# Kernel optimization log

Hardware: AMD Instinct MI355X
Metric: run time of the kernel (lower is better)

## Reference

```python
import jax, jax.numpy as jnp
import numpy as np

EPS = 1e-6

def _normalize(A):
    # zero the diagonal, add self-loops
    n = A.shape[-1]
    eye = jnp.eye(n, dtype=A.dtype)
    A_hat = A * (1.0 - eye) + eye  # [B,N,N]
    # symmetric degree normalization with eps inside as in the TF code:
    # d = 1/(eps + sqrt(rowsum)); norm = diag(d) @ A_hat @ diag(d)
    d = 1.0 / (EPS + jnp.sqrt(jnp.sum(A_hat, axis=2)))  # [B,N]
    return A_hat * d[:, :, None] * d[:, None, :]


def setup_inputs() -> dict:
    key = jax.random.key(0)
    k1, k2, k3 = jax.random.split(key, 3)
    B, N, F, O = 8, 2048, 128, 128
    x = jax.random.normal(k1, (B, N, F), dtype=jnp.float32)
    adj = jax.random.uniform(k2, (B, N, N), dtype=jnp.float32)
    kernel = jax.random.normal(k3, (F, O), dtype=jnp.float32) * 0.05
    return {"x": x, "adj": adj, "kernel": kernel}


def reference(x, adj, kernel):
    norm = _normalize(adj)                      # [B,N,N]
    agg = jnp.einsum('bnm,bmf->bnf', norm, x)   # batch_dot
    out = jnp.einsum('bnf,fo->bno', agg, kernel)
    return jax.nn.relu(out)
```

## Files before the change

kernel.cpp:

```cpp
#include <hip/hip_runtime.h>


typedef __bf16 bf16x8 __attribute__((ext_vector_type(8)));
typedef float  f32x4  __attribute__((ext_vector_type(4)));

#define NN 2048
#define NB 8

__device__ __forceinline__ void load_lds16(__bf16* lds, const __bf16* g) {
    __builtin_amdgcn_global_load_lds(
        (const __attribute__((address_space(1))) void*)g,
        (__attribute__((address_space(3))) void*)lds, 16, 0, 0);
}

__global__ __launch_bounds__(256) void d_kernel(const float* __restrict__ adj,
                                                float* __restrict__ dvec,
                                                const float* __restrict__ W,
                                                __bf16* __restrict__ Wt) {
    if (blockIdx.x >= NB * NN / 4) {
        int idx = (blockIdx.x - NB * NN / 4) * 256 + threadIdx.x;
        int f = idx >> 7, o = idx & 127;
        Wt[o * 128 + f] = (__bf16)W[idx];
        return;
    }
    const int lane = threadIdx.x & 63;
    const int row  = blockIdx.x * 4 + (threadIdx.x >> 6);
    const float* rp = adj + (size_t)row * NN;
    float4 s4 = {0.f, 0.f, 0.f, 0.f};
#pragma unroll
    for (int it = 0; it < 8; ++it) {
        float4 v = *(const float4*)(rp + it * 256 + lane * 4);
        s4.x += v.x; s4.y += v.y; s4.z += v.z; s4.w += v.w;
    }
    float s = (s4.x + s4.y) + (s4.z + s4.w);
#pragma unroll
    for (int off = 32; off; off >>= 1) s += __shfl_down(s, off);
    if (lane == 0) {
        int n = row & (NN - 1);
        float sh = s - rp[n] + 1.0f;
        dvec[row] = 1.0f / (1e-6f + sqrtf(sh));
    }
}

__global__ __launch_bounds__(256) void xw_kernel(const float* __restrict__ x,
                                                 const __bf16* __restrict__ Wt,
                                                 const float* __restrict__ dvec,
                                                 __bf16* __restrict__ yt) {
    const int lane = threadIdx.x & 63;
    const int wave = threadIdx.x >> 6;
    const int b    = blockIdx.x & 7;
    const int mt   = (blockIdx.x >> 3) * 4 + wave;
    const int m0   = mt * 16;
    const int kgrp = (lane >> 4) * 8;
    const float* xp = x + ((size_t)b * NN + m0 + (lane & 15)) * 128 + kgrp;

    f32x4 acc[8];
#pragma unroll
    for (int i = 0; i < 8; ++i) acc[i] = (f32x4){0.f, 0.f, 0.f, 0.f};

#pragma unroll
    for (int kt = 0; kt < 4; ++kt) {
        f32x4 a0 = *(const f32x4*)(xp + kt * 32);
        f32x4 a1 = *(const f32x4*)(xp + kt * 32 + 4);
        float av[8] = {a0.x, a0.y, a0.z, a0.w, a1.x, a1.y, a1.z, a1.w};
        bf16x8 af;
#pragma unroll
        for (int j = 0; j < 8; ++j) af[j] = (__bf16)av[j];
#pragma unroll
        for (int nb = 0; nb < 8; ++nb) {
            bf16x8 bfv = *(const bf16x8*)(Wt + (nb * 16 + (lane & 15)) * 128 +
                                          kt * 32 + kgrp);
            acc[nb] = __builtin_amdgcn_mfma_f32_16x16x32_bf16(af, bfv, acc[nb], 0, 0, 0);
        }
    }
    const int col0 = lane & 15;
    const int rq   = (lane >> 4) * 4;
#pragma unroll
    for (int r = 0; r < 4; ++r) {
        int m = m0 + rq + r;
        float dm = dvec[b * NN + m];
#pragma unroll
        for (int nb = 0; nb < 8; ++nb) {
            int o = nb * 16 + col0;
            yt[((size_t)b * 128 + o) * NN + m] = (__bf16)(acc[nb][r] * dm);
        }
    }
}

__global__ __launch_bounds__(256) void gemm_kernel(const float* __restrict__ adj,
                                                   const __bf16* __restrict__ yt,
                                                   const float* __restrict__ dvec,
                                                   float* __restrict__ out) {
    __shared__ alignas(16) __bf16 sB[2][128][32];

    const int tid  = threadIdx.x;
    const int wave = tid >> 6;
    const int lane = tid & 63;
    const int b    = blockIdx.x & 7;
    const int tile = blockIdx.x >> 3;
    const int rsel = (wave & 1) * 16;
    const int csel = (wave >> 1) * 64;
    const int kgrp = (lane >> 4) * 8;

    const int arow_loc = tile * 32 + rsel + (lane & 15);
    const float* ap = adj + ((size_t)b * NN + arow_loc) * NN + kgrp;

    const __bf16* ytb = yt + (size_t)b * 128 * NN;
    const int b_row0 = wave * 32;
    const __bf16* b_src = ytb + (size_t)(b_row0 + (lane >> 2)) * NN + (lane & 3) * 8;

    f32x4 acc[4];
#pragma unroll
    for (int i = 0; i < 4; ++i) acc[i] = (f32x4){0.f, 0.f, 0.f, 0.f};

    load_lds16(&sB[0][b_row0][0], b_src);
    load_lds16(&sB[0][b_row0 + 16][0], b_src + (size_t)16 * NN);
    __builtin_amdgcn_sched_barrier(0);
    f32x4 ca0 = *(const f32x4*)(ap);
    f32x4 ca1 = *(const f32x4*)(ap + 4);

    for (int kt = 0; kt < 64; ++kt) {
        const int cur = kt & 1;
        asm volatile("s_waitcnt vmcnt(2)" ::: "memory");
        __builtin_amdgcn_sched_barrier(0);
        __builtin_amdgcn_s_barrier();
        __builtin_amdgcn_sched_barrier(0);

        f32x4 na0, na1;
        if (kt + 1 < 64) {
            const __bf16* bs = b_src + (size_t)(kt + 1) * 32;
            load_lds16(&sB[cur ^ 1][b_row0][0], bs);
            load_lds16(&sB[cur ^ 1][b_row0 + 16][0], bs + (size_t)16 * NN);
            __builtin_amdgcn_sched_barrier(0);
            na0 = *(const f32x4*)(ap + (kt + 1) * 32);
            na1 = *(const f32x4*)(ap + (kt + 1) * 32 + 4);
        }

        bf16x8 af;
        af[0] = (__bf16)ca0.x; af[1] = (__bf16)ca0.y;
        af[2] = (__bf16)ca0.z; af[3] = (__bf16)ca0.w;
        af[4] = (__bf16)ca1.x; af[5] = (__bf16)ca1.y;
        af[6] = (__bf16)ca1.z; af[7] = (__bf16)ca1.w;

#pragma unroll
        for (int nb = 0; nb < 4; ++nb) {
            bf16x8 bfv = *(const bf16x8*)(
                &sB[cur][csel + nb * 16 + (lane & 15)][kgrp]);
            acc[nb] = __builtin_amdgcn_mfma_f32_16x16x32_bf16(af, bfv, acc[nb], 0, 0, 0);
        }
        ca0 = na0; ca1 = na1;
    }

    const int col0 = lane & 15;
    const int rq   = (lane >> 4) * 4;
#pragma unroll
    for (int r = 0; r < 4; ++r) {
        int n_loc = tile * 32 + rsel + rq + r;
        size_t grow = (size_t)b * NN + n_loc;
        float dn   = dvec[grow];
        float cfac = 1.0f - adj[grow * NN + n_loc];
#pragma unroll
        for (int nb = 0; nb < 4; ++nb) {
            int o = csel + nb * 16 + col0;
            float yp = (float)ytb[(size_t)o * NN + n_loc];
            float v = (acc[nb][r] + cfac * yp) * dn;
            out[grow * 128 + o] = v > 0.f ? v : 0.f;
        }
    }
}

extern "C" void kernel_launch(void* const* d_in, const int* in_sizes, int n_in,
                              void* d_out, int out_size, void* d_ws, size_t ws_size,
                              hipStream_t stream) {
    const float* x   = (const float*)d_in[0];
    const float* adj = (const float*)d_in[1];
    const float* W   = (const float*)d_in[2];
    float* out = (float*)d_out;

    char* ws = (char*)d_ws;
    float*  dvec = (float*)ws;
    __bf16* Wt   = (__bf16*)(ws + (64 << 10));
    __bf16* yt   = (__bf16*)(ws + (128 << 10));

    hipLaunchKernelGGL(d_kernel, dim3(NB * NN / 4 + 64), dim3(256), 0, stream,
                       adj, dvec, W, Wt);
    hipLaunchKernelGGL(xw_kernel, dim3(256), dim3(256), 0, stream, x, Wt, dvec, yt);
    hipLaunchKernelGGL(gemm_kernel, dim3(512), dim3(256), 0, stream,
                       adj, yt, dvec, out);
}
```

Before: 246.5 us.

## Deepen gemm pipeline to 4-stage LDS ring with 2-ahead A prefetch

The main GEMM loop moves from a double-buffered LDS scheme to a 4-slot ring that issues B tile loads three iterations ahead and A register loads two iterations ahead. The loop is manually unrolled by two so the A prefetch registers alternate, and the waitcnt thresholds are tuned for the tail iterations. The intent is to keep more memory requests in flight and hide global latency behind MFMA work, at the cost of more LDS and registers per block.

```diff
diff --git a/kernel.cpp b/kernel.cpp
--- a/kernel.cpp
+++ b/kernel.cpp
@@ -87,11 +87,46 @@
     }
 }
 
+
+#define GBODY(KT, S, DO_A, DO_G, WAITSTR)                                    \
+  do {                                                                       \
+    asm volatile("s_waitcnt vmcnt(" WAITSTR ")" ::: "memory");               \
+    __builtin_amdgcn_sched_barrier(0);                                       \
+    __builtin_amdgcn_s_barrier();                                            \
+    __builtin_amdgcn_sched_barrier(0);                                       \
+    const int cur_ = (KT) & 3;                                               \
+    bf16x8 bv0 = *(const bf16x8*)(&sB[cur_][csel +  0 + l15][kgrp]);         \
+    bf16x8 bv1 = *(const bf16x8*)(&sB[cur_][csel + 16 + l15][kgrp]);         \
+    bf16x8 bv2 = *(const bf16x8*)(&sB[cur_][csel + 32 + l15][kgrp]);         \
+    bf16x8 bv3 = *(const bf16x8*)(&sB[cur_][csel + 48 + l15][kgrp]);         \
+    bf16x8 af;                                                               \
+    af[0] = (__bf16)pa0_##S.x; af[1] = (__bf16)pa0_##S.y;                    \
+    af[2] = (__bf16)pa0_##S.z; af[3] = (__bf16)pa0_##S.w;                    \
+    af[4] = (__bf16)pa1_##S.x; af[5] = (__bf16)pa1_##S.y;                    \
+    af[6] = (__bf16)pa1_##S.z; af[7] = (__bf16)pa1_##S.w;                    \
+    __builtin_amdgcn_sched_barrier(0);                                       \
+    if (DO_A) {                                                              \
+      pa0_##S = *(const f32x4*)(ap + ((KT) + 2) * 32);                       \
+      pa1_##S = *(const f32x4*)(ap + ((KT) + 2) * 32 + 4);                   \
+    }                                                                        \
+    __builtin_amdgcn_sched_barrier(0);                                       \
+    if (DO_G) {                                                              \
+      const __bf16* bs_ = b_src + (size_t)((KT) + 3) * 32;                   \
+      load_lds16(&sB[((KT) + 3) & 3][b_row0][0], bs_);                       \
+      load_lds16(&sB[((KT) + 3) & 3][b_row0 + 16][0], bs_ + (size_t)16 * NN);\
+    }                                                                        \
+    __builtin_amdgcn_sched_barrier(0);                                       \
+    acc[0] = __builtin_amdgcn_mfma_f32_16x16x32_bf16(af, bv0, acc[0], 0, 0, 0); \
+    acc[1] = __builtin_amdgcn_mfma_f32_16x16x32_bf16(af, bv1, acc[1], 0, 0, 0); \
+    acc[2] = __builtin_amdgcn_mfma_f32_16x16x32_bf16(af, bv2, acc[2], 0, 0, 0); \
+    acc[3] = __builtin_amdgcn_mfma_f32_16x16x32_bf16(af, bv3, acc[3], 0, 0, 0); \
+  } while (0)
+
 __global__ __launch_bounds__(256) void gemm_kernel(const float* __restrict__ adj,
                                                    const __bf16* __restrict__ yt,
                                                    const float* __restrict__ dvec,
                                                    float* __restrict__ out) {
-    __shared__ alignas(16) __bf16 sB[2][128][32];
+    __shared__ alignas(16) __bf16 sB[4][128][32];
 
     const int tid  = threadIdx.x;
     const int wave = tid >> 6;
@@ -101,8 +136,9 @@
     const int rsel = (wave & 1) * 16;
     const int csel = (wave >> 1) * 64;
     const int kgrp = (lane >> 4) * 8;
-
-    const int arow_loc = tile * 32 + rsel + (lane & 15);
+    const int l15  = lane & 15;
+
+    const int arow_loc = tile * 32 + rsel + l15;
     const float* ap = adj + ((size_t)b * NN + arow_loc) * NN + kgrp;
 
     const __bf16* ytb = yt + (size_t)b * 128 * NN;
@@ -113,46 +149,34 @@
 #pragma unroll
     for (int i = 0; i < 4; ++i) acc[i] = (f32x4){0.f, 0.f, 0.f, 0.f};
 
+    f32x4 pa0_0, pa1_0, pa0_1, pa1_1;
+
     load_lds16(&sB[0][b_row0][0], b_src);
     load_lds16(&sB[0][b_row0 + 16][0], b_src + (size_t)16 * NN);
     __builtin_amdgcn_sched_barrier(0);
-    f32x4 ca0 = *(const f32x4*)(ap);
-    f32x4 ca1 = *(const f32x4*)(ap + 4);
-
-    for (int kt = 0; kt < 64; ++kt) {
-        const int cur = kt & 1;
-        asm volatile("s_waitcnt vmcnt(2)" ::: "memory");
-        __builtin_amdgcn_sched_barrier(0);
-        __builtin_amdgcn_s_barrier();
-        __builtin_amdgcn_sched_barrier(0);
-
-        f32x4 na0, na1;
-        if (kt + 1 < 64) {
-            const __bf16* bs = b_src + (size_t)(kt + 1) * 32;
-            load_lds16(&sB[cur ^ 1][b_row0][0], bs);
-            load_lds16(&sB[cur ^ 1][b_row0 + 16][0], bs + (size_t)16 * NN);
-            __builtin_amdgcn_sched_barrier(0);
-            na0 = *(const f32x4*)(ap + (kt + 1) * 32);
-            na1 = *(const f32x4*)(ap + (kt + 1) * 32 + 4);
-        }
-
-        bf16x8 af;
-        af[0] = (__bf16)ca0.x; af[1] = (__bf16)ca0.y;
-        af[2] = (__bf16)ca0.z; af[3] = (__bf16)ca0.w;
-        af[4] = (__bf16)ca1.x; af[5] = (__bf16)ca1.y;
-        af[6] = (__bf16)ca1.z; af[7] = (__bf16)ca1.w;
-
-#pragma unroll
-        for (int nb = 0; nb < 4; ++nb) {
-            bf16x8 bfv = *(const bf16x8*)(
-                &sB[cur][csel + nb * 16 + (lane & 15)][kgrp]);
-            acc[nb] = __builtin_amdgcn_mfma_f32_16x16x32_bf16(af, bfv, acc[nb], 0, 0, 0);
-        }
-        ca0 = na0; ca1 = na1;
-    }
-
-    const int col0 = lane & 15;
-    const int rq   = (lane >> 4) * 4;
+    pa0_0 = *(const f32x4*)(ap);
+    pa1_0 = *(const f32x4*)(ap + 4);
+    __builtin_amdgcn_sched_barrier(0);
+    load_lds16(&sB[1][b_row0][0], b_src + 32);
+    load_lds16(&sB[1][b_row0 + 16][0], b_src + (size_t)16 * NN + 32);
+    __builtin_amdgcn_sched_barrier(0);
+    pa0_1 = *(const f32x4*)(ap + 32);
+    pa1_1 = *(const f32x4*)(ap + 36);
+    __builtin_amdgcn_sched_barrier(0);
+    load_lds16(&sB[2][b_row0][0], b_src + 64);
+    load_lds16(&sB[2][b_row0 + 16][0], b_src + (size_t)16 * NN + 64);
+    __builtin_amdgcn_sched_barrier(0);
+
+    for (int kt = 0; kt < 60; kt += 2) {
+        GBODY(kt,     0, 1, 1, "6");
+        GBODY(kt + 1, 1, 1, 1, "6");
+    }
+    GBODY(60, 0, 1, 1, "6");
+    GBODY(61, 1, 1, 0, "6");
+    GBODY(62, 0, 0, 0, "4");
+    GBODY(63, 1, 0, 0, "0");
+
+    const int rq = (lane >> 4) * 4;
 #pragma unroll
     for (int r = 0; r < 4; ++r) {
         int n_loc = tile * 32 + rsel + rq + r;
@@ -161,7 +185,7 @@
         float cfac = 1.0f - adj[grow * NN + n_loc];
 #pragma unroll
         for (int nb = 0; nb < 4; ++nb) {
-            int o = csel + nb * 16 + col0;
+            int o = csel + nb * 16 + l15;
             float yp = (float)ytb[(size_t)o * NN + n_loc];
             float v = (acc[nb][r] + cfac * yp) * dn;
             out[grow * 128 + o] = v > 0.f ? v : 0.f;
```

After: 244.7 us. Within noise of the previous version (-0.7%).
